# Optimization experiments

Hardware: AMD Instinct MI355X
Metric: run time of the kernel (lower is better)

## Reference

```python
import jax, jax.numpy as jnp
import numpy as np

L, B, T, C, H, V = 4, 4, 1024, 1024, 16, 32000
DH = C // H
FF = 4 * C
IGNORE = 5
EPS = 1e-5


def setup_inputs() -> dict:
    key = jax.random.key(0)
    ks = jax.random.split(key, 12)
    s = 0.02
    return {
        "idx": jax.random.randint(ks[0], (B, T), 0, V),
        "targets": jax.random.randint(ks[1], (B, T), 0, V),
        "tok_emb": jax.random.normal(ks[2], (V, C), jnp.float32) * s,
        "pos_emb": jax.random.normal(ks[3], (T, C), jnp.float32) * s,
        "Wq": jax.random.normal(ks[4], (L, C, C), jnp.float32) * s,
        "Wk": jax.random.normal(ks[5], (L, C, C), jnp.float32) * s,
        "Wv": jax.random.normal(ks[6], (L, C, C), jnp.float32) * s,
        "Wo": jax.random.normal(ks[7], (L, C, C), jnp.float32) * s,
        "bo": jnp.zeros((L, C), jnp.float32),
        "ln1_g": jnp.ones((L, C), jnp.float32),
        "ln1_b": jnp.zeros((L, C), jnp.float32),
        "ln2_g": jnp.ones((L, C), jnp.float32),
        "ln2_b": jnp.zeros((L, C), jnp.float32),
        "W1": jax.random.normal(ks[8], (L, C, FF), jnp.float32) * s,
        "b1": jnp.zeros((L, FF), jnp.float32),
        "W2": jax.random.normal(ks[9], (L, FF, C), jnp.float32) * s,
        "b2": jnp.zeros((L, C), jnp.float32),
        "lnf_g": jnp.ones((C,), jnp.float32),
        "lnf_b": jnp.zeros((C,), jnp.float32),
        "Whead": jax.random.normal(ks[10], (C, V), jnp.float32) * s,
        "bhead": jnp.zeros((V,), jnp.float32),
    }


def _layernorm(x, g, b):
    mu = jnp.mean(x, axis=-1, keepdims=True)
    var = jnp.var(x, axis=-1, keepdims=True)
    return (x - mu) * jax.lax.rsqrt(var + EPS) * g + b


def _gpt_forward(idx, targets, tok_emb, pos_emb, Wq, Wk, Wv, Wo, bo,
                 ln1_g, ln1_b, ln2_g, ln2_b, W1, b1, W2, b2,
                 lnf_g, lnf_b, Whead, bhead):
    x = tok_emb[idx] + pos_emb[None, :, :]  # [B,T,C]
    causal = jnp.tril(jnp.ones((T, T), bool))
    for i in range(L):
        h = _layernorm(x, ln1_g[i], ln1_b[i])
        q = (h @ Wq[i]).reshape(B, T, H, DH)
        k = (h @ Wk[i]).reshape(B, T, H, DH)
        v = (h @ Wv[i]).reshape(B, T, H, DH)
        wei = jnp.einsum("bqhd,bkhd->bhqk", q, k) * (DH ** -0.5)
        wei = jnp.where(causal[None, None], wei, -jnp.inf)
        wei = jax.nn.softmax(wei, axis=-1)
        att = jnp.einsum("bhqk,bkhd->bqhd", wei, v).reshape(B, T, C)
        x = x + att @ Wo[i] + bo[i]
        h = _layernorm(x, ln2_g[i], ln2_b[i])
        x = x + jax.nn.gelu(h @ W1[i] + b1[i], approximate=False) @ W2[i] + b2[i]
    x = _layernorm(x, lnf_g, lnf_b)
    logits = x @ Whead + bhead  # [B,T,V]
    # cross-entropy with ignore_index=5
    lg = logits.reshape(B * T, V)
    tg = targets.reshape(B * T)
    logp = jax.nn.log_softmax(lg, axis=-1)
    nll = -jnp.take_along_axis(logp, tg[:, None], axis=-1)[:, 0]
    valid = (tg != IGNORE).astype(lg.dtype)
    loss = jnp.sum(nll * valid) / jnp.maximum(jnp.sum(valid), 1.0)
    return logits, loss


def reference(idx, targets, tok_emb, pos_emb, Wq, Wk, Wv, Wo, bo,
              ln1_g, ln1_b, ln2_g, ln2_b, W1, b1, W2, b2,
              lnf_g, lnf_b, Whead, bhead):
    return _gpt_forward(idx, targets, tok_emb, pos_emb, Wq, Wk, Wv, Wo, bo,
                        ln1_g, ln1_b, ln2_g, ln2_b, W1, b1, W2, b2,
                        lnf_g, lnf_b, Whead, bhead)
```

## Files before the change

kernel.cpp:

```cpp
#include <hip/hip_runtime.h>
#include <cstdint>
#include <cstddef>

#define Lx 4
#define Bx 4
#define Tx 1024
#define Cx 1024
#define Hx 16
#define DHx 64
#define FFx 4096
#define Vx 32000
#define BTx 4096

typedef __attribute__((ext_vector_type(8))) __bf16 bf16x8;
typedef __attribute__((ext_vector_type(4))) float f32x4;
typedef __attribute__((ext_vector_type(8))) short short8;

__device__ __forceinline__ float bflo(unsigned u){ return __builtin_bit_cast(float, u << 16); }
__device__ __forceinline__ float bfhi(unsigned u){ return __builtin_bit_cast(float, u & 0xffff0000u); }
__device__ __forceinline__ float bf2f(short s){ return bflo((unsigned)(unsigned short)s); }
__device__ __forceinline__ short f2bf(float f){
  unsigned u = __builtin_bit_cast(unsigned, f);
  u += 0x7fffu + ((u >> 16) & 1u);
  return (short)(u >> 16);
}

__device__ __forceinline__ void gload_lds16(const short* g, short* l){
  __builtin_amdgcn_global_load_lds(
      (const __attribute__((address_space(1))) unsigned int*)g,
      (__attribute__((address_space(3))) unsigned int*)l, 16, 0, 0);
}

__device__ __forceinline__ int xcd_swizzle(int orig, int nwg){
  const int q = nwg >> 3, r = nwg & 7;
  const int xcd = orig & 7, wg = orig >> 3;
  const int base = (xcd < r) ? xcd * (q + 1) : r * (q + 1) + (xcd - r) * q;
  return base + wg;
}

__global__ __launch_bounds__(256) void embed_kernel(
    const int* __restrict__ idx, const float* __restrict__ tok,
    const float* __restrict__ pos, float* __restrict__ x)
{
  const int bt = blockIdx.x;
  const int t  = bt & (Tx - 1);
  const int tid = threadIdx.x;
  const int tk = idx[bt];
  float4 a = *(const float4*)&tok[((size_t)tk << 10) + (tid << 2)];
  const float4 p = *(const float4*)&pos[((size_t)t << 10) + (tid << 2)];
  a.x += p.x; a.y += p.y; a.z += p.z; a.w += p.w;
  *(float4*)&x[((size_t)bt << 10) + (tid << 2)] = a;
}

__global__ __launch_bounds__(256) void ln_kernel(
    const float* __restrict__ x, const float* __restrict__ g,
    const float* __restrict__ b, short* __restrict__ out)
{
  const int row = blockIdx.x;
  const int tid = threadIdx.x;
  const float4 v = *(const float4*)&x[((size_t)row << 10) + (tid << 2)];
  float s  = v.x + v.y + v.z + v.w;
  float ss = v.x*v.x + v.y*v.y + v.z*v.z + v.w*v.w;
  #pragma unroll
  for (int off = 32; off >= 1; off >>= 1) {
    s  += __shfl_down(s, off);
    ss += __shfl_down(ss, off);
  }
  __shared__ float rs[4], rss[4];
  const int lane = tid & 63, w = tid >> 6;
  if (lane == 0) { rs[w] = s; rss[w] = ss; }
  __syncthreads();
  s  = rs[0] + rs[1] + rs[2] + rs[3];
  ss = rss[0] + rss[1] + rss[2] + rss[3];
  const float mu  = s * (1.0f / Cx);
  const float var = ss * (1.0f / Cx) - mu * mu;
  const float rstd = rsqrtf(var + 1e-5f);
  const float4 g4 = *(const float4*)&g[tid << 2];
  const float4 b4 = *(const float4*)&b[tid << 2];
  short4 o;
  o.x = f2bf((v.x - mu) * rstd * g4.x + b4.x);
  o.y = f2bf((v.y - mu) * rstd * g4.y + b4.y);
  o.z = f2bf((v.z - mu) * rstd * g4.z + b4.z);
  o.w = f2bf((v.w - mu) * rstd * g4.w + b4.w);
  *(short4*)&out[((size_t)row << 10) + (tid << 2)] = o;
}

__global__ __launch_bounds__(256) void wconv_kernel(
    const float* __restrict__ W, short* __restrict__ Wt, int K, int N)
{
  __shared__ float tile[32][33];
  const int n0 = blockIdx.x << 5, k0 = blockIdx.y << 5;
  const int tx = threadIdx.x & 31, ty = threadIdx.x >> 5;
  #pragma unroll
  for (int r = 0; r < 4; ++r)
    tile[ty + (r << 3)][tx] = __builtin_nontemporal_load(
        &W[(size_t)(k0 + ty + (r << 3)) * N + n0 + tx]);
  __syncthreads();
  #pragma unroll
  for (int r = 0; r < 4; ++r)
    Wt[(size_t)(n0 + ty + (r << 3)) * K + k0 + tx] = f2bf(tile[tx][ty + (r << 3)]);
}

__global__ __launch_bounds__(256) void wconv4_kernel(
    const float* __restrict__ Wq, const float* __restrict__ Wk,
    const float* __restrict__ Wv, const float* __restrict__ Wo,
    short* __restrict__ qkvT, short* __restrict__ woT)
{
  __shared__ float tile[32][33];
  const int z = blockIdx.z;
  const float* W = (z == 0) ? Wq : (z == 1) ? Wk : (z == 2) ? Wv : Wo;
  short* Wt = (z < 3) ? qkvT + (size_t)z * Cx * Cx : woT;
  const int n0 = blockIdx.x << 5, k0 = blockIdx.y << 5;
  const int tx = threadIdx.x & 31, ty = threadIdx.x >> 5;
  #pragma unroll
  for (int r = 0; r < 4; ++r)
    tile[ty + (r << 3)][tx] = __builtin_nontemporal_load(
        &W[(size_t)(k0 + ty + (r << 3)) * Cx + n0 + tx]);
  __syncthreads();
  #pragma unroll
  for (int r = 0; r < 4; ++r)
    Wt[(size_t)(n0 + ty + (r << 3)) * Cx + k0 + tx] = f2bf(tile[tx][ty + (r << 3)]);
}

template<int MODE>
__global__ __launch_bounds__(256) void gemm_kernel(
    const short* __restrict__ A, const short* __restrict__ Bt,
    const float* __restrict__ bias, const float* __restrict__ res,
    float* __restrict__ outF, short* __restrict__ outB, int N, int K)
{
  __shared__ __align__(16) short sA[128 * 32];
  __shared__ __align__(16) short sB[128 * 32];
  const int tid  = threadIdx.x;
  const int lane = tid & 63;
  const int wave = tid >> 6;
  const int bid  = xcd_swizzle((int)blockIdx.x, (int)gridDim.x);
  const int tm = (bid & 31) << 7;
  const int tn = (bid >> 5) << 7;
  const int wm = ((wave >> 1) & 1) << 6;
  const int wn = (wave & 1) << 6;

  f32x4 acc[4][4] = {};

  const int o1  = tid << 4;
  const int row = o1 >> 6;
  const int col = (o1 & 63) >> 1;
  const short* gA1 = A  + (size_t)(tm + row) * K + col;
  const short* gA2 = A  + (size_t)(tm + row + 64) * K + col;
  const short* gB1 = Bt + (size_t)(tn + row) * K + col;
  const short* gB2 = Bt + (size_t)(tn + row + 64) * K + col;
  short* lA1 = sA + (wave << 9);
  short* lA2 = sA + 2048 + (wave << 9);
  short* lB1 = sB + (wave << 9);
  short* lB2 = sB + 2048 + (wave << 9);

  for (int k0 = 0; k0 < K; k0 += 32) {
    gload_lds16(gA1 + k0, lA1);
    gload_lds16(gA2 + k0, lA2);
    gload_lds16(gB1 + k0, lB1);
    gload_lds16(gB2 + k0, lB2);
    __syncthreads();
    bf16x8 aF[4], bF[4];
    const int kb = (lane >> 4) << 3;
    const int rsel = lane & 15;
    #pragma unroll
    for (int m = 0; m < 4; ++m)
      aF[m] = *(const bf16x8*)&sA[(wm + m * 16 + rsel) * 32 + kb];
    #pragma unroll
    for (int n = 0; n < 4; ++n)
      bF[n] = *(const bf16x8*)&sB[(wn + n * 16 + rsel) * 32 + kb];
    #pragma unroll
    for (int m = 0; m < 4; ++m) {
      #pragma unroll
      for (int n = 0; n < 4; ++n)
        acc[m][n] = __builtin_amdgcn_mfma_f32_16x16x32_bf16(aF[m], bF[n], acc[m][n], 0, 0, 0);
    }
    __syncthreads();
  }

  const int r0 = (lane >> 4) << 2;
  const int c0 = lane & 15;
  #pragma unroll
  for (int m = 0; m < 4; ++m) {
    #pragma unroll
    for (int n = 0; n < 4; ++n) {
      #pragma unroll
      for (int r = 0; r < 4; ++r) {
        const int grow = tm + wm + m * 16 + r0 + r;
        const int gcol = tn + wn + n * 16 + c0;
        const float v = acc[m][n][r];
        if constexpr (MODE == 0) {
          const int which = gcol >> 10;
          const int cc = gcol & 1023;
          const int b = grow >> 10, t = grow & 1023;
          const int hh = cc >> 6, d = cc & 63;
          outB[(size_t)which * (BTx * Cx) +
               ((size_t)((((b << 4) + hh) << 10) + t) << 6) + d] = f2bf(v);
        } else {
          const size_t o = (size_t)grow * N + gcol;
          outF[o] = res[o] + v + bias[gcol];
        }
      }
    }
  }
}

#define GBAR() do { __builtin_amdgcn_sched_barrier(0); __builtin_amdgcn_s_barrier(); __builtin_amdgcn_sched_barrier(0); } while(0)
#define VM4 asm volatile("s_waitcnt vmcnt(4)" ::: "memory");
#define NOWAIT

#define PHASE(qq, dd, STAGES, ENDW) do { \
  aF[0][0] = RD_A(dd, qq, 0, 0); aF[0][1] = RD_A(dd, qq, 0, 1); \
  aF[1][0] = RD_A(dd, qq, 1, 0); aF[1][1] = RD_A(dd, qq, 1, 1); \
  STAGES \
  GBAR(); \
  asm volatile("s_waitcnt lgkmcnt(0)" ::: "memory"); \
  __builtin_amdgcn_sched_barrier(0); \
  __builtin_amdgcn_s_setprio(1); \
  _Pragma("unroll") \
  for (int ks = 0; ks < 2; ++ks) { \
    _Pragma("unroll") \
    for (int mf = 0; mf < 2; ++mf) { \
      _Pragma("unroll") \
      for (int nf = 0; nf < 4; ++nf) \
        acc[((qq) << 1) + mf][nf] = __builtin_amdgcn_mfma_f32_16x16x32_bf16( \
            aF[mf][ks], bF[nf][ks], acc[((qq) << 1) + mf][nf], 0, 0, 0); \
    } \
  } \
  __builtin_amdgcn_s_setprio(0); \
  ENDW \
  GBAR(); \
} while (0)

#define BLOAD(dd) do { \
  _Pragma("unroll") \
  for (int nf = 0; nf < 4; ++nf) { bF[nf][0] = RD_B(dd, nf, 0); bF[nf][1] = RD_B(dd, nf, 1); } \
} while (0)

template<int MODE>
__global__ __launch_bounds__(512, 2) void gemm256_kernel(
    const short* __restrict__ A, const short* __restrict__ Bt,
    const float* __restrict__ bias, float* __restrict__ outF,
    short* __restrict__ outB, float* __restrict__ cep, int N, int K)
{
  __shared__ __align__(16) char lds[131072];
  const int tid  = threadIdx.x;
  const int lane = tid & 63;
  const int wid  = tid >> 6;
  const int wm   = wid >> 2;
  const int wn   = wid & 3;
  const int r15  = lane & 15;
  const int g4   = lane >> 4;
  const int bid  = xcd_swizzle((int)blockIdx.x, (int)gridDim.x);
  const int tm   = (bid & 15) << 8;
  const int tn   = (bid >> 4) << 8;
  const int NT   = K >> 6;
  const int NI   = NT >> 1;

  const int row0   = tid >> 3;
  const int innerE = ((tid & 7) ^ ((tid >> 3) & 7)) << 3;
  const int X0     = tid << 4;
  const short* srcA = A  + (size_t)(tm + row0) * K + innerE;
  const short* srcB = Bt + (size_t)(tn + row0) * K + innerE;
  const size_t h128K = (size_t)128 * K;
  const size_t r64K  = (size_t)64 * K;

  auto STAGE_A = [&](int t, int hh) {
    const short* s = srcA + (size_t)hh * h128K + (t << 6);
    char* d = lds + ((t & 1) << 15) + (hh << 14) + X0;
    gload_lds16(s, (short*)d);
    gload_lds16(s + r64K, (short*)(d + 8192));
  };
  auto STAGE_B = [&](int t, int hh) {
    const short* s = srcB + (size_t)hh * h128K + (t << 6);
    char* d = lds + 65536 + ((t & 1) << 15) + (hh << 14) + X0;
    gload_lds16(s, (short*)d);
    gload_lds16(s + r64K, (short*)(d + 8192));
  };

  const int arowb = (wm << 7) + r15;
  const int bcolb = (wn << 6) + r15;
  const int kchnk = g4 << 4;
  auto RD_A = [&](int d, int q, int mf, int ks) -> bf16x8 {
    const int row = arowb + (q << 5) + (mf << 4);
    return *(const bf16x8*)(lds + (d << 15) + (row << 7) +
                            ((((ks) << 6) + kchnk) ^ ((row & 7) << 4)));
  };
  auto RD_B = [&](int d, int nf, int ks) -> bf16x8 {
    const int colc = bcolb + (nf << 4);
    return *(const bf16x8*)(lds + 65536 + (d << 15) + (colc << 7) +
                            ((((ks) << 6) + kchnk) ^ ((colc & 7) << 4)));
  };

  f32x4 acc[8][4] = {};

  STAGE_A(0, 0); STAGE_A(0, 1); STAGE_B(0, 0); STAGE_B(0, 1);
  STAGE_B(1, 0); STAGE_B(1, 1);
  VM4
  GBAR();

  for (int i = 0; i < NI; ++i) {
    const int t1 = 2 * i + 1;
    const int ta = (2 * i + 2 < NT) ? 2 * i + 2 : NT - 2;
    const int tb = (2 * i + 3 < NT) ? 2 * i + 3 : NT - 1;
    bf16x8 aF[2][2], bF[4][2];
    BLOAD(0);
    PHASE(0, 0, { STAGE_A(t1, 0); },                  NOWAIT);
    PHASE(1, 0, { STAGE_A(t1, 1); STAGE_B(ta, 0); },  NOWAIT);
    PHASE(2, 0, { STAGE_B(ta, 1); },                  NOWAIT);
    PHASE(3, 0, { },                                  VM4);
    BLOAD(1);
    PHASE(0, 1, { STAGE_A(ta, 0); },                  NOWAIT);
    PHASE(1, 1, { STAGE_A(ta, 1); STAGE_B(tb, 0); },  NOWAIT);
    PHASE(2, 1, { STAGE_B(tb, 1); },                  NOWAIT);
    PHASE(3, 1, { },                                  VM4);
  }

  if constexpr (MODE == 3) {
    const int nb = tn >> 8;
    float bb4[4];
    #pragma unroll
    for (int nf = 0; nf < 4; ++nf) bb4[nf] = bias[tn + (wn << 6) + (nf << 4) + r15];
    #pragma unroll
    for (int m8 = 0; m8 < 8; ++m8)
      #pragma unroll
      for (int nf = 0; nf < 4; ++nf)
        #pragma unroll
        for (int r = 0; r < 4; ++r) acc[m8][nf][r] += bb4[nf];

    #pragma unroll
    for (int m8 = 0; m8 < 8; ++m8) {
      #pragma unroll
      for (int nf = 0; nf < 4; ++nf) {
        #pragma unroll
        for (int r = 0; r < 4; ++r) {
          const int grow = tm + (wm << 7) + (m8 << 4) + (g4 << 2) + r;
          const int gcol = tn + (wn << 6) + (nf << 4) + r15;
          outF[(size_t)grow * N + gcol] = acc[m8][nf][r];
        }
      }
    }

    float* cepart = (float*)lds;
    #pragma unroll
    for (int m8 = 0; m8 < 8; ++m8) {
      #pragma unroll
      for (int r = 0; r < 4; ++r) {
        float sm = __expf(acc[m8][0][r]) + __expf(acc[m8][1][r])
                 + __expf(acc[m8][2][r]) + __expf(acc[m8][3][r]);
        sm += __shfl_xor(sm, 1);
        sm += __shfl_xor(sm, 2);
        sm += __shfl_xor(sm, 4);
        sm += __shfl_xor(sm, 8);
        if (r15 == 0)
          cepart[(wn << 8) + (wm << 7) + (m8 << 4) + (g4 << 2) + r] = sm;
      }
    }
    __syncthreads();
    if (tid < 256) {
      const float S = cepart[tid] + cepart[256 + tid] + cepart[512 + tid] + cepart[768 + tid];
      cep[(size_t)(tm + tid) * 125 + nb] = S;
    }
  } else {
    float bb4[4];
    #pragma unroll
    for (int nf = 0; nf < 4; ++nf) bb4[nf] = bias[tn + (wn << 6) + (nf << 4) + r15];
    #pragma unroll
    for (int m8 = 0; m8 < 8; ++m8) {
      #pragma unroll
      for (int nf = 0; nf < 4; ++nf) {
        #pragma unroll
        for (int r = 0; r < 4; ++r) {
          const int grow = tm + (wm << 7) + (m8 << 4) + (g4 << 2) + r;
          const int gcol = tn + (wn << 6) + (nf << 4) + r15;
          const float t2 = acc[m8][nf][r] + bb4[nf];
          const float gl = 0.5f * t2 * (1.0f + erff(t2 * 0.7071067811865475f));
          outB[(size_t)grow * N + gcol] = f2bf(gl);
        }
      }
    }
  }
}

__global__ __launch_bounds__(256) void fattn_kernel(
    const short* __restrict__ q, const short* __restrict__ k,
    const short* __restrict__ v, short* __restrict__ att)
{
  __shared__ __align__(16) short sQ[4096];
  __shared__ __align__(16) short sK[2][4096];
  __shared__ __align__(16) short sVT[2][4096];
  __shared__ __align__(16) short sP[4][1024];

  const int tid  = threadIdx.x;
  const int lane = tid & 63;
  const int w    = tid >> 6;
  const int r15  = lane & 15;
  const int g4   = lane >> 4;
  const int bid  = xcd_swizzle((int)blockIdx.x, (int)gridDim.x);
  const int qt   = bid & 15;
  const int bh   = bid >> 4;

  const char* Qb = (const char*)(q + ((size_t)bh << 16)) + ((size_t)qt << 13);
  const char* Kb = (const char*)(k + ((size_t)bh << 16));
  const char* Vb = (const char*)(v + ((size_t)bh << 16));

  const int X0  = tid << 4;
  const int X1  = X0 + 4096;
  const int sw0 = X0 ^ (((X0 >> 7) & 7) << 4);
  const int sw1 = X1 ^ (((X1 >> 7) & 7) << 4);
  const int ldsOff0 = (w << 10);
  const int ldsOff1 = (w << 10) + 4096;

  const int vdh  = (lane & 31) << 1;
  const int vkv0 = (((w << 1) + (lane >> 5)) << 3);
  const int vb0  = (vdh * 128 + vkv0 * 2)       ^ ((vdh & 7) << 4);
  const int vb1  = ((vdh + 1) * 128 + vkv0 * 2) ^ (((vdh + 1) & 7) << 4);

  auto loadV = [&](int kt, unsigned* uv) {
    const char* Vt = Vb + ((size_t)kt << 13);
    #pragma unroll
    for (int j = 0; j < 8; ++j)
      uv[j] = *(const unsigned*)(Vt + ((vkv0 + j) << 7) + (vdh << 1));
  };
  auto writeV = [&](int buf, const unsigned* uv) {
    short8 plo, phi;
    #pragma unroll
    for (int j = 0; j < 8; ++j) {
      plo[j] = (short)(uv[j] & 0xffffu);
      phi[j] = (short)(uv[j] >> 16);
    }
    *(short8*)((char*)sVT[buf] + vb0) = plo;
    *(short8*)((char*)sVT[buf] + vb1) = phi;
  };
  auto stageK = [&](int kt, int buf) {
    const char* Kt = Kb + ((size_t)kt << 13);
    gload_lds16((const short*)(Kt + sw0), (short*)((char*)sK[buf] + ldsOff0));
    gload_lds16((const short*)(Kt + sw1), (short*)((char*)sK[buf] + ldsOff1));
  };

  gload_lds16((const short*)(Qb + sw0), (short*)((char*)sQ + ldsOff0));
  gload_lds16((const short*)(Qb + sw1), (short*)((char*)sQ + ldsOff1));
  stageK(0, 0);
  {
    unsigned uv[8];
    loadV(0, uv);
    writeV(0, uv);
  }
  __syncthreads();

  bf16x8 aQ[2];
  {
    const int qrow = (w << 4) + r15;
    const int base = qrow * 128 + (g4 << 4);
    const int sz = (qrow & 7) << 4;
    aQ[0] = *(const bf16x8*)((char*)sQ + ((base     ) ^ sz));
    aQ[1] = *(const bf16x8*)((char*)sQ + ((base + 64) ^ sz));
  }

  float m[4] = {-3e38f, -3e38f, -3e38f, -3e38f};
  float l[4] = {0.f, 0.f, 0.f, 0.f};
  f32x4 acc_o[4] = {};
  const int qrow_g0 = (qt << 6) + (w << 4) + (g4 << 2);

  for (int kt = 0; kt <= qt; ++kt) {
    const int cur = kt & 1;
    unsigned uv2[8];
    if (kt < qt) {
      stageK(kt + 1, cur ^ 1);
      loadV(kt + 1, uv2);
    }

    f32x4 s[4] = {};
    #pragma unroll
    for (int f = 0; f < 4; ++f) {
      const int kv = (f << 4) + r15;
      const int kb = kv * 128 + (g4 << 4);
      const int sz = (kv & 7) << 4;
      const bf16x8 b0 = *(const bf16x8*)((char*)sK[cur] + ((kb     ) ^ sz));
      const bf16x8 b1 = *(const bf16x8*)((char*)sK[cur] + ((kb + 64) ^ sz));
      s[f] = __builtin_amdgcn_mfma_f32_16x16x32_bf16(aQ[0], b0, s[f], 0, 0, 0);
      s[f] = __builtin_amdgcn_mfma_f32_16x16x32_bf16(aQ[1], b1, s[f], 0, 0, 0);
    }
    #pragma unroll
    for (int f = 0; f < 4; ++f) {
      #pragma unroll
      for (int r = 0; r < 4; ++r) {
        float sv = s[f][r] * 0.125f;
        if ((kt << 6) + (f << 4) + r15 > qrow_g0 + r) sv = -3e38f;
        s[f][r] = sv;
      }
    }
    #pragma unroll
    for (int r = 0; r < 4; ++r) {
      float mx = fmaxf(fmaxf(s[0][r], s[1][r]), fmaxf(s[2][r], s[3][r]));
      mx = fmaxf(mx, __shfl_xor(mx, 1));
      mx = fmaxf(mx, __shfl_xor(mx, 2));
      mx = fmaxf(mx, __shfl_xor(mx, 4));
      mx = fmaxf(mx, __shfl_xor(mx, 8));
      const float mn = fmaxf(m[r], mx);
      const float e  = __expf(m[r] - mn);
      float sum = 0.f;
      #pragma unroll
      for (int f = 0; f < 4; ++f) {
        const float p = __expf(s[f][r] - mn);
        s[f][r] = p; sum += p;
      }
      sum += __shfl_xor(sum, 1);
      sum += __shfl_xor(sum, 2);
      sum += __shfl_xor(sum, 4);
      sum += __shfl_xor(sum, 8);
      l[r] = l[r] * e + sum;
      m[r] = mn;
      acc_o[0][r] *= e; acc_o[1][r] *= e; acc_o[2][r] *= e; acc_o[3][r] *= e;
    }
    short* Pw = sP[w];
    #pragma unroll
    for (int f = 0; f < 4; ++f) {
      #pragma unroll
      for (int r = 0; r < 4; ++r) {
        const int prow = (g4 << 2) + r;
        const int byte = prow * 128 + (((f << 4) + r15) << 1);
        *(short*)((char*)Pw + (byte ^ ((prow & 7) << 4))) = f2bf(s[f][r]);
      }
    }
    #pragma unroll
    for (int ks = 0; ks < 2; ++ks) {
      const int ab = r15 * 128 + (ks << 6) + (g4 << 4);
      const bf16x8 aP = *(const bf16x8*)((char*)Pw + (ab ^ ((r15 & 7) << 4)));
      #pragma unroll
      for (int f = 0; f < 4; ++f) {
        const int dh = (f << 4) + r15;
        const int bb = dh * 128 + (ks << 6) + (g4 << 4);
        const bf16x8 bV = *(const bf16x8*)((char*)sVT[cur] + (bb ^ ((dh & 7) << 4)));
        acc_o[f] = __builtin_amdgcn_mfma_f32_16x16x32_bf16(aP, bV, acc_o[f], 0, 0, 0);
      }
    }

    if (kt < qt) writeV(cur ^ 1, uv2);
    __syncthreads();
  }

  const int b = bh >> 4, hh = bh & 15;
  #pragma unroll
  for (int f = 0; f < 4; ++f) {
    #pragma unroll
    for (int r = 0; r < 4; ++r) {
      const int qg = qrow_g0 + r;
      const int dh = (f << 4) + r15;
      att[((size_t)((b << 10) + qg) << 10) + (hh << 6) + dh] = f2bf(acc_o[f][r] / l[r]);
    }
  }
}

__global__ __launch_bounds__(256) void ce_lse_kernel(
    const float* __restrict__ part, const float* __restrict__ logits,
    const int* __restrict__ tgt, float2* __restrict__ nll)
{
  const int row  = blockIdx.x * 4 + (threadIdx.x >> 6);
  const int lane = threadIdx.x & 63;
  float S = 0.f;
  #pragma unroll
  for (int p = 0; p < 2; ++p) {
    const int i = lane + (p << 6);
    if (i < 125) S += part[(size_t)row * 125 + i];
  }
  #pragma unroll
  for (int off = 32; off >= 1; off >>= 1) S += __shfl_xor(S, off);
  if (lane == 0) {
    const int tg = tgt[row];
    float v = 0.f, cnt = 0.f;
    if (tg != 5) {
      const float lt = logits[(size_t)row * Vx + tg];
      v = -(lt - logf(S));
      cnt = 1.f;
    }
    float2 o2; o2.x = v; o2.y = cnt;
    nll[row] = o2;
  }
}

__global__ __launch_bounds__(256) void ce_sum_kernel(
    const float2* __restrict__ nll, float* __restrict__ out)
{
  const int tid = threadIdx.x;
  float s = 0.f, c = 0.f;
  #pragma unroll
  for (int i = 0; i < 16; ++i) {
    const float2 v = nll[tid * 16 + i];
    s += v.x; c += v.y;
  }
  __shared__ float ls[256], lc[256];
  ls[tid] = s; lc[tid] = c;
  __syncthreads();
  for (int off = 128; off >= 1; off >>= 1) {
    if (tid < off) { ls[tid] += ls[tid + off]; lc[tid] += lc[tid + off]; }
    __syncthreads();
  }
  if (tid == 0) out[131072000ull] = ls[0] / fmaxf(lc[0], 1.0f);
}

extern "C" void kernel_launch(void* const* d_in, const int* in_sizes, int n_in,
                              void* d_out, int out_size, void* d_ws, size_t ws_size,
                              hipStream_t stream)
{
  const int*   idx     = (const int*)d_in[0];
  const int*   targets = (const int*)d_in[1];
  const float* tok_emb = (const float*)d_in[2];
  const float* pos_emb = (const float*)d_in[3];
  const float* Wq      = (const float*)d_in[4];
  const float* Wk      = (const float*)d_in[5];
  const float* Wv      = (const float*)d_in[6];
  const float* Wo      = (const float*)d_in[7];
  const float* bo      = (const float*)d_in[8];
  const float* ln1_g   = (const float*)d_in[9];
  const float* ln1_b   = (const float*)d_in[10];
  const float* ln2_g   = (const float*)d_in[11];
  const float* ln2_b   = (const float*)d_in[12];
  const float* W1      = (const float*)d_in[13];
  const float* b1      = (const float*)d_in[14];
  const float* W2      = (const float*)d_in[15];
  const float* b2      = (const float*)d_in[16];
  const float* lnf_g   = (const float*)d_in[17];
  const float* lnf_b   = (const float*)d_in[18];
  const float* Whead   = (const float*)d_in[19];
  const float* bhead   = (const float*)d_in[20];
  float* out = (float*)d_out;

  char* ws = (char*)d_ws;
  size_t off = 0;
  auto alloc = [&](size_t bytes) -> char* {
    char* p = ws + off;
    off += (bytes + 255) & ~(size_t)255;
    return p;
  };
  float* x    = (float*)alloc((size_t)BTx * Cx * 4);
  short* h    = (short*)alloc((size_t)BTx * Cx * 2);
  char*  blk  = ws + off;
  short* qb   = (short*)alloc((size_t)BTx * Cx * 2);
  short* kb   = (short*)alloc((size_t)BTx * Cx * 2);
  short* vb   = (short*)alloc((size_t)BTx * Cx * 2);
  short* attb = (short*)alloc((size_t)BTx * Cx * 2);
  short* ffb  = (short*)alloc((size_t)BTx * FFx * 2);
  short* wheadT = (short*)blk;
  short* wqkvT = (short*)alloc((size_t)3 * Cx * Cx * 2);
  short* woT  = (short*)alloc((size_t)Cx * Cx * 2);
  short* w1T  = (short*)alloc((size_t)Cx * FFx * 2);
  short* w2T  = (short*)alloc((size_t)FFx * Cx * 2);
  if (ws_size < off) return;
  float* part  = (float*)wqkvT;
  float2* nllb = (float2*)woT;

  embed_kernel<<<BTx, 256, 0, stream>>>(idx, tok_emb, pos_emb, x);

  for (int i = 0; i < Lx; ++i) {
    const size_t wo_off = (size_t)i * Cx * Cx;
    const size_t w1_off = (size_t)i * Cx * FFx;
    wconv4_kernel<<<dim3(Cx / 32, Cx / 32, 4), 256, 0, stream>>>(
        Wq + wo_off, Wk + wo_off, Wv + wo_off, Wo + wo_off, wqkvT, woT);
    wconv_kernel<<<dim3(FFx / 32, Cx / 32), 256, 0, stream>>>(W1 + w1_off, w1T, Cx, FFx);
    wconv_kernel<<<dim3(Cx / 32, FFx / 32), 256, 0, stream>>>(W2 + w1_off, w2T, FFx, Cx);

    ln_kernel<<<BTx, 256, 0, stream>>>(x, ln1_g + i * Cx, ln1_b + i * Cx, h);
    gemm_kernel<0><<<32 * 24, 256, 0, stream>>>(h, wqkvT, nullptr, nullptr, nullptr, qb, 3 * Cx, Cx);
    fattn_kernel<<<Bx * Hx * (Tx / 64), 256, 0, stream>>>(qb, kb, vb, attb);
    gemm_kernel<1><<<32 * 8, 256, 0, stream>>>(attb, woT, bo + i * Cx, x, x, nullptr, Cx, Cx);

    ln_kernel<<<BTx, 256, 0, stream>>>(x, ln2_g + i * Cx, ln2_b + i * Cx, h);
    gemm256_kernel<2><<<16 * 16, 512, 0, stream>>>(h, w1T, b1 + i * FFx, nullptr, ffb, nullptr, FFx, Cx);
    gemm_kernel<1><<<32 * 8, 256, 0, stream>>>(ffb, w2T, b2 + i * Cx, x, x, nullptr, Cx, FFx);
  }

  ln_kernel<<<BTx, 256, 0, stream>>>(x, lnf_g, lnf_b, h);
  wconv_kernel<<<dim3(Vx / 32, Cx / 32), 256, 0, stream>>>(Whead, wheadT, Cx, Vx);
  gemm256_kernel<3><<<16 * 125, 512, 0, stream>>>(h, wheadT, bhead, out, nullptr, part, Vx, Cx);

  ce_lse_kernel<<<BTx / 4, 256, 0, stream>>>(part, out, targets, nllb);
  ce_sum_kernel<<<1, 256, 0, stream>>>(nllb, out);
}
```

Baseline: 1.541 ms.

## Peel last GEMM iteration to overlap epilogue; widen flash-attention blocks to 128 queries

The 256-tile GEMM now peels its final K iteration. It drops redundant prefetches and writes each quarter of the accumulator (bias, GELU or logits store) right after that quarter's last MFMAs, so the epilogue overlaps with the remaining compute. Separately, the flash-attention kernel goes from 64 to 128 query rows per block with 512 threads. Each K/V tile is staged once for twice as many queries and the V transpose loads use 16-bit elements. This cuts K/V reload traffic and block count, but leaves fewer blocks and coarser causal load balance.

```diff
diff --git a/kernel.cpp b/kernel.cpp
--- a/kernel.cpp
+++ b/kernel.cpp
@@ -17,7 +17,6 @@
 typedef __attribute__((ext_vector_type(8))) short short8;
 
 __device__ __forceinline__ float bflo(unsigned u){ return __builtin_bit_cast(float, u << 16); }
-__device__ __forceinline__ float bfhi(unsigned u){ return __builtin_bit_cast(float, u & 0xffff0000u); }
 __device__ __forceinline__ float bf2f(short s){ return bflo((unsigned)(unsigned short)s); }
 __device__ __forceinline__ short f2bf(float f){
   unsigned u = __builtin_bit_cast(unsigned, f);
@@ -206,6 +205,7 @@
 
 #define GBAR() do { __builtin_amdgcn_sched_barrier(0); __builtin_amdgcn_s_barrier(); __builtin_amdgcn_sched_barrier(0); } while(0)
 #define VM4 asm volatile("s_waitcnt vmcnt(4)" ::: "memory");
+#define VM0 asm volatile("s_waitcnt vmcnt(0)" ::: "memory");
 #define NOWAIT
 
 #define PHASE(qq, dd, STAGES, ENDW) do { \
@@ -236,6 +236,28 @@
   for (int nf = 0; nf < 4; ++nf) { bF[nf][0] = RD_B(dd, nf, 0); bF[nf][1] = RD_B(dd, nf, 1); } \
 } while (0)
 
+#define FINISH(qq) do { \
+  _Pragma("unroll") \
+  for (int m8 = ((qq) << 1); m8 < ((qq) << 1) + 2; ++m8) { \
+    _Pragma("unroll") \
+    for (int nf = 0; nf < 4; ++nf) { \
+      _Pragma("unroll") \
+      for (int r = 0; r < 4; ++r) { \
+        const int grow = tm + (wm << 7) + (m8 << 4) + (g4 << 2) + r; \
+        const int gcol = tn + (wn << 6) + (nf << 4) + r15; \
+        if constexpr (MODE == 3) { \
+          acc[m8][nf][r] += bb4[nf]; \
+          outF[(size_t)grow * N + gcol] = acc[m8][nf][r]; \
+        } else { \
+          const float t2 = acc[m8][nf][r] + bb4[nf]; \
+          const float gl = 0.5f * t2 * (1.0f + erff(t2 * 0.7071067811865475f)); \
+          outB[(size_t)grow * N + gcol] = f2bf(gl); \
+        } \
+      } \
+    } \
+  } \
+} while (0)
+
 template<int MODE>
 __global__ __launch_bounds__(512, 2) void gemm256_kernel(
     const short* __restrict__ A, const short* __restrict__ Bt,
@@ -298,10 +320,10 @@
   VM4
   GBAR();
 
-  for (int i = 0; i < NI; ++i) {
+  for (int i = 0; i < NI - 1; ++i) {
     const int t1 = 2 * i + 1;
-    const int ta = (2 * i + 2 < NT) ? 2 * i + 2 : NT - 2;
-    const int tb = (2 * i + 3 < NT) ? 2 * i + 3 : NT - 1;
+    const int ta = 2 * i + 2;
+    const int tb = 2 * i + 3;
     bf16x8 aF[2][2], bF[4][2];
     BLOAD(0);
     PHASE(0, 0, { STAGE_A(t1, 0); },                  NOWAIT);
@@ -315,31 +337,26 @@
     PHASE(3, 1, { },                                  VM4);
   }
 
+  float bb4[4];
+  #pragma unroll
+  for (int nf = 0; nf < 4; ++nf) bb4[nf] = bias[tn + (wn << 6) + (nf << 4) + r15];
+
+  {
+    bf16x8 aF[2][2], bF[4][2];
+    BLOAD(0);
+    PHASE(0, 0, { STAGE_A(NT - 1, 0); }, NOWAIT);
+    PHASE(1, 0, { STAGE_A(NT - 1, 1); }, NOWAIT);
+    PHASE(2, 0, { },                     NOWAIT);
+    PHASE(3, 0, { },                     VM0);
+    BLOAD(1);
+    PHASE(0, 1, { }, NOWAIT); FINISH(0);
+    PHASE(1, 1, { }, NOWAIT); FINISH(1);
+    PHASE(2, 1, { }, NOWAIT); FINISH(2);
+    PHASE(3, 1, { }, NOWAIT); FINISH(3);
+  }
+
   if constexpr (MODE == 3) {
     const int nb = tn >> 8;
-    float bb4[4];
-    #pragma unroll
-    for (int nf = 0; nf < 4; ++nf) bb4[nf] = bias[tn + (wn << 6) + (nf << 4) + r15];
-    #pragma unroll
-    for (int m8 = 0; m8 < 8; ++m8)
-      #pragma unroll
-      for (int nf = 0; nf < 4; ++nf)
-        #pragma unroll
-        for (int r = 0; r < 4; ++r) acc[m8][nf][r] += bb4[nf];
-
-    #pragma unroll
-    for (int m8 = 0; m8 < 8; ++m8) {
-      #pragma unroll
-      for (int nf = 0; nf < 4; ++nf) {
-        #pragma unroll
-        for (int r = 0; r < 4; ++r) {
-          const int grow = tm + (wm << 7) + (m8 << 4) + (g4 << 2) + r;
-          const int gcol = tn + (wn << 6) + (nf << 4) + r15;
-          outF[(size_t)grow * N + gcol] = acc[m8][nf][r];
-        }
-      }
-    }
-
     float* cepart = (float*)lds;
     #pragma unroll
     for (int m8 = 0; m8 < 8; ++m8) {
@@ -360,35 +377,17 @@
       const float S = cepart[tid] + cepart[256 + tid] + cepart[512 + tid] + cepart[768 + tid];
       cep[(size_t)(tm + tid) * 125 + nb] = S;
     }
-  } else {
-    float bb4[4];
-    #pragma unroll
-    for (int nf = 0; nf < 4; ++nf) bb4[nf] = bias[tn + (wn << 6) + (nf << 4) + r15];
-    #pragma unroll
-    for (int m8 = 0; m8 < 8; ++m8) {
-      #pragma unroll
-      for (int nf = 0; nf < 4; ++nf) {
-        #pragma unroll
-        for (int r = 0; r < 4; ++r) {
-          const int grow = tm + (wm << 7) + (m8 << 4) + (g4 << 2) + r;
-          const int gcol = tn + (wn << 6) + (nf << 4) + r15;
-          const float t2 = acc[m8][nf][r] + bb4[nf];
-          const float gl = 0.5f * t2 * (1.0f + erff(t2 * 0.7071067811865475f));
-          outB[(size_t)grow * N + gcol] = f2bf(gl);
-        }
-      }
-    }
-  }
-}
-
-__global__ __launch_bounds__(256) void fattn_kernel(
+  }
+}
+
+__global__ __launch_bounds__(512) void fattn_kernel(
     const short* __restrict__ q, const short* __restrict__ k,
     const short* __restrict__ v, short* __restrict__ att)
 {
-  __shared__ __align__(16) short sQ[4096];
+  __shared__ __align__(16) short sQ[8192];
   __shared__ __align__(16) short sK[2][4096];
   __shared__ __align__(16) short sVT[2][4096];
-  __shared__ __align__(16) short sP[4][1024];
+  __shared__ __align__(16) short sP[8][1024];
 
   const int tid  = threadIdx.x;
   const int lane = tid & 63;
@@ -396,52 +395,45 @@
   const int r15  = lane & 15;
   const int g4   = lane >> 4;
   const int bid  = xcd_swizzle((int)blockIdx.x, (int)gridDim.x);
-  const int qt   = bid & 15;
-  const int bh   = bid >> 4;
-
-  const char* Qb = (const char*)(q + ((size_t)bh << 16)) + ((size_t)qt << 13);
+  const int qb   = bid & 7;
+  const int bh   = bid >> 3;
+
+  const char* Qb = (const char*)(q + ((size_t)bh << 16)) + ((size_t)qb << 14);
   const char* Kb = (const char*)(k + ((size_t)bh << 16));
   const char* Vb = (const char*)(v + ((size_t)bh << 16));
 
   const int X0  = tid << 4;
-  const int X1  = X0 + 4096;
   const int sw0 = X0 ^ (((X0 >> 7) & 7) << 4);
+  const int X1  = X0 + 8192;
   const int sw1 = X1 ^ (((X1 >> 7) & 7) << 4);
-  const int ldsOff0 = (w << 10);
-  const int ldsOff1 = (w << 10) + 4096;
-
-  const int vdh  = (lane & 31) << 1;
-  const int vkv0 = (((w << 1) + (lane >> 5)) << 3);
-  const int vb0  = (vdh * 128 + vkv0 * 2)       ^ ((vdh & 7) << 4);
-  const int vb1  = ((vdh + 1) * 128 + vkv0 * 2) ^ (((vdh + 1) & 7) << 4);
-
-  auto loadV = [&](int kt, unsigned* uv) {
-    const char* Vt = Vb + ((size_t)kt << 13);
-    #pragma unroll
-    for (int j = 0; j < 8; ++j)
-      uv[j] = *(const unsigned*)(Vt + ((vkv0 + j) << 7) + (vdh << 1));
-  };
-  auto writeV = [&](int buf, const unsigned* uv) {
-    short8 plo, phi;
-    #pragma unroll
-    for (int j = 0; j < 8; ++j) {
-      plo[j] = (short)(uv[j] & 0xffffu);
-      phi[j] = (short)(uv[j] >> 16);
-    }
-    *(short8*)((char*)sVT[buf] + vb0) = plo;
-    *(short8*)((char*)sVT[buf] + vb1) = phi;
-  };
+  const int ldsW = (w << 10);
+
+  const int vdh  = tid & 63;
+  const int vkv0 = (tid >> 6) << 3;
+  const int vb0  = (vdh * 128 + vkv0 * 2) ^ ((vdh & 7) << 4);
+
   auto stageK = [&](int kt, int buf) {
     const char* Kt = Kb + ((size_t)kt << 13);
-    gload_lds16((const short*)(Kt + sw0), (short*)((char*)sK[buf] + ldsOff0));
-    gload_lds16((const short*)(Kt + sw1), (short*)((char*)sK[buf] + ldsOff1));
-  };
-
-  gload_lds16((const short*)(Qb + sw0), (short*)((char*)sQ + ldsOff0));
-  gload_lds16((const short*)(Qb + sw1), (short*)((char*)sQ + ldsOff1));
+    gload_lds16((const short*)(Kt + sw0), (short*)((char*)sK[buf] + ldsW));
+  };
+  auto loadV = [&](int kt, unsigned short* uv) {
+    const char* Vt = Vb + ((size_t)kt << 13);
+    #pragma unroll
+    for (int j = 0; j < 8; ++j)
+      uv[j] = *(const unsigned short*)(Vt + ((vkv0 + j) << 7) + (vdh << 1));
+  };
+  auto writeV = [&](int buf, const unsigned short* uv) {
+    short8 p;
+    #pragma unroll
+    for (int j = 0; j < 8; ++j) p[j] = (short)uv[j];
+    *(short8*)((char*)sVT[buf] + vb0) = p;
+  };
+
+  gload_lds16((const short*)(Qb + sw0), (short*)((char*)sQ + ldsW));
+  gload_lds16((const short*)(Qb + sw1), (short*)((char*)sQ + ldsW + 8192));
   stageK(0, 0);
   {
-    unsigned uv[8];
+    unsigned short uv[8];
     loadV(0, uv);
     writeV(0, uv);
   }
@@ -459,12 +451,13 @@
   float m[4] = {-3e38f, -3e38f, -3e38f, -3e38f};
   float l[4] = {0.f, 0.f, 0.f, 0.f};
   f32x4 acc_o[4] = {};
-  const int qrow_g0 = (qt << 6) + (w << 4) + (g4 << 2);
-
-  for (int kt = 0; kt <= qt; ++kt) {
+  const int qrow_g0 = (qb << 7) + (w << 4) + (g4 << 2);
+  const int ktmax = 2 * qb + 1;
+
+  for (int kt = 0; kt <= ktmax; ++kt) {
     const int cur = kt & 1;
-    unsigned uv2[8];
-    if (kt < qt) {
+    unsigned short uv2[8];
+    if (kt < ktmax) {
       stageK(kt + 1, cur ^ 1);
       loadV(kt + 1, uv2);
     }
@@ -535,7 +528,7 @@
       }
     }
 
-    if (kt < qt) writeV(cur ^ 1, uv2);
+    if (kt < ktmax) writeV(cur ^ 1, uv2);
     __syncthreads();
   }
 
@@ -661,7 +654,7 @@
 
     ln_kernel<<<BTx, 256, 0, stream>>>(x, ln1_g + i * Cx, ln1_b + i * Cx, h);
     gemm_kernel<0><<<32 * 24, 256, 0, stream>>>(h, wqkvT, nullptr, nullptr, nullptr, qb, 3 * Cx, Cx);
-    fattn_kernel<<<Bx * Hx * (Tx / 64), 256, 0, stream>>>(qb, kb, vb, attb);
+    fattn_kernel<<<Bx * Hx * (Tx / 128), 512, 0, stream>>>(qb, kb, vb, attb);
     gemm_kernel<1><<<32 * 8, 256, 0, stream>>>(attb, woT, bo + i * Cx, x, x, nullptr, Cx, Cx);
 
     ln_kernel<<<BTx, 256, 0, stream>>>(x, ln2_g + i * Cx, ln2_b + i * Cx, h);
```

After: 1.621 ms. 1.05x slower.
